# Kernel tuning notes

Hardware: AMD Instinct MI355X
Metric: run time of the kernel (lower is better)

Reference implementation:

```python
import jax, jax.numpy as jnp
import numpy as np
import math

B, L, D_MODEL, H = 2, 2048, 2048, 16
HD = D_MODEL // H  # 128


def _rope(x):
    # x: (B,H,L,HD) interleaved-pair RoPE (GPT-NeoX / RoFormer style with ::2 strides)
    hd = x.shape[-1]
    inv_freq = 1.0 / (10000.0 ** (jnp.arange(0, hd, 2, dtype=jnp.float32) / hd))  # (HD/2,)
    t = jnp.arange(x.shape[2], dtype=jnp.float32)
    freqs = t[:, None] * inv_freq[None, :]            # (L, HD/2)
    cos = jnp.cos(freqs)[None, None]                  # (1,1,L,HD/2)
    sin = jnp.sin(freqs)[None, None]
    x1 = x[..., ::2]
    x2 = x[..., 1::2]
    even = x1 * cos - x2 * sin
    odd = x1 * sin + x2 * cos
    # interleave even/odd back: (...,HD/2,2) -> (...,HD)
    return jnp.stack([even, odd], axis=-1).reshape(x.shape)


def setup_inputs() -> dict:
    key = jax.random.key(0)
    k1, k2, k3, k4, k5, k6 = jax.random.split(key, 6)
    x_q = jax.random.normal(k1, (B, L, D_MODEL), dtype=jnp.float32)
    x_kv = jax.random.normal(k2, (B, L, D_MODEL), dtype=jnp.float32)
    # causal additive mask: 0 keep, -1e9 masked, broadcastable to (B,H,L,S)
    causal = jnp.tril(jnp.ones((L, L), dtype=bool))
    attn_mask = jnp.where(causal, 0.0, -1e9).astype(jnp.float32)[None, None]
    s = 0.02
    w_q = jax.random.normal(k3, (D_MODEL, D_MODEL), dtype=jnp.float32) * s
    w_k = jax.random.normal(k4, (D_MODEL, D_MODEL), dtype=jnp.float32) * s
    w_v = jax.random.normal(k5, (D_MODEL, D_MODEL), dtype=jnp.float32) * s
    w_o = jax.random.normal(k6, (D_MODEL, D_MODEL), dtype=jnp.float32) * s
    return {"x_q": x_q, "x_kv": x_kv, "attn_mask": attn_mask,
            "w_q": w_q, "w_k": w_k, "w_v": w_v, "w_o": w_o}


def _shape(x):
    b, l, _ = x.shape
    return x.reshape(b, l, H, HD).transpose(0, 2, 1, 3)  # (B,H,L,HD)


def reference(x_q, x_kv, attn_mask, w_q, w_k, w_v, w_o):
    # torch Linear (no bias): y = x @ W.T
    q = _shape(x_q @ w_q.T)
    k = _shape(x_kv @ w_k.T)
    v = _shape(x_kv @ w_v.T)
    q = _rope(q)
    k = _rope(k)
    scale = 1.0 / math.sqrt(HD)
    scores = jnp.einsum('bhld,bhsd->bhls', q, k) * scale + attn_mask
    attn = jax.nn.softmax(scores, axis=-1)            # (B,H,L,S)
    out = jnp.einsum('bhls,bhsd->bhld', attn, v)
    out = out.transpose(0, 2, 1, 3).reshape(x_q.shape[0], x_q.shape[1], H * HD)
    out = out @ w_o.T
    return (out, attn)
```

## Files before the change

kernel.cpp:

```cpp
#include <hip/hip_runtime.h>
#include <hip/hip_bf16.h>
#include <math.h>

#define B_ 2
#define L_ 2048
#define D_ 2048
#define H_ 16
#define HD_ 128
#define E_ (B_*L_*D_)
#define W_ (D_*D_)

typedef __bf16 bf16;
typedef __bf16 bf16x8 __attribute__((ext_vector_type(8)));
typedef __bf16 bf16x4 __attribute__((ext_vector_type(4)));
typedef float  f32x4  __attribute__((ext_vector_type(4)));

#define GLL16(gp_, lp_) __builtin_amdgcn_global_load_lds( \
    (const __attribute__((address_space(1))) void*)(gp_), \
    (__attribute__((address_space(3))) void*)(lp_), 16, 0, 0)

#define BARRIER() do { asm volatile("" ::: "memory"); \
    __builtin_amdgcn_s_barrier(); \
    asm volatile("" ::: "memory"); } while (0)

#define WAITN(N) asm volatile("s_waitcnt vmcnt(" #N ")" ::: "memory")

__global__ void prep(const float* __restrict__ xq, const float* __restrict__ xkv,
                     const float* __restrict__ wq, const float* __restrict__ wk,
                     const float* __restrict__ wv, const float* __restrict__ wo,
                     bf16* __restrict__ xqb, bf16* __restrict__ xkvb,
                     bf16* __restrict__ wqb, bf16* __restrict__ wkb,
                     bf16* __restrict__ wvb, bf16* __restrict__ wob,
                     float* __restrict__ ct, float* __restrict__ st) {
  int g = blockIdx.x;
  if (g < 16384) {
    const float* s = (g < 8192) ? xq : xkv;
    bf16* d = (g < 8192) ? xqb : xkvb;
    int i = ((g & 8191) * 256 + threadIdx.x) * 4;
    f32x4 v = *reinterpret_cast<const f32x4*>(s + i);
    bf16x4 o; o[0]=(bf16)v[0]; o[1]=(bf16)v[1]; o[2]=(bf16)v[2]; o[3]=(bf16)v[3];
    *reinterpret_cast<bf16x4*>(d + i) = o;
  } else if (g < 32768) {
    int gg = g - 16384;
    int which = gg >> 12;
    const float* s = (which==0)?wq:(which==1)?wk:(which==2)?wv:wo;
    bf16* d = (which==0)?wqb:(which==1)?wkb:(which==2)?wvb:wob;
    int i = ((gg & 4095) * 256 + threadIdx.x) * 4;
    f32x4 v = *reinterpret_cast<const f32x4*>(s + i);
    bf16x4 o; o[0]=(bf16)v[0]; o[1]=(bf16)v[1]; o[2]=(bf16)v[2]; o[3]=(bf16)v[3];
    *reinterpret_cast<bf16x4*>(d + i) = o;
  } else {
    int idx = (g - 32768) * 256 + threadIdx.x;
    int t = idx >> 6, i = idx & 63;
    float inv = powf(10000.0f, -2.0f * (float)i / 128.0f);
    float f = (float)t * inv;
    ct[t * 64 + i] = cosf(f);
    st[t * 64 + i] = sinf(f);
  }
}

__global__ __launch_bounds__(256, 4) void gemm_qkv(
    const bf16* __restrict__ xq, const bf16* __restrict__ xkv,
    const bf16* __restrict__ wq, const bf16* __restrict__ wk, const bf16* __restrict__ wv,
    const float* __restrict__ ct, const float* __restrict__ st,
    bf16* __restrict__ Qo, bf16* __restrict__ Ko, bf16* __restrict__ Vt) {
  __shared__ bf16 As[128 * 64];
  __shared__ bf16 Bs[128 * 64];
  const int tid = threadIdx.x;
  const int lane = tid & 63;
  const int w = tid >> 6;
  const int l15 = lane & 15, lg = lane >> 4;
  const int which = blockIdx.x >> 4;
  const int n0 = (blockIdx.x & 15) * 128;
  const int m0 = blockIdx.y * 128;
  const int wm = (w >> 1) * 64, wn = (w & 1) * 64;
  const bf16* A  = (which == 0) ? xq : xkv;
  const bf16* Wt = (which == 0) ? wq : ((which == 1) ? wk : wv);

  int rowS[4], schS[4];
#pragma unroll
  for (int s = 0; s < 4; ++s) {
    int cl = s * 256 + tid;
    rowS[s] = cl >> 3;
    schS[s] = ((cl & 7) ^ ((cl >> 3) & 7)) << 3;
  }

  f32x4 acc[4][4];
#pragma unroll
  for (int m = 0; m < 4; ++m)
#pragma unroll
    for (int n = 0; n < 4; ++n) acc[m][n] = (f32x4){0.f, 0.f, 0.f, 0.f};

  for (int kt = 0; kt < D_; kt += 64) {
    __syncthreads();
#pragma unroll
    for (int s = 0; s < 4; ++s) {
      GLL16(A  + (size_t)(m0 + rowS[s]) * D_ + kt + schS[s], As + s * 2048 + w * 512);
      GLL16(Wt + (size_t)(n0 + rowS[s]) * D_ + kt + schS[s], Bs + s * 2048 + w * 512);
    }
    __syncthreads();
#pragma unroll
    for (int kk = 0; kk < 64; kk += 32) {
      bf16x8 af[4], bfr[4];
#pragma unroll
      for (int m = 0; m < 4; ++m)
        af[m] = *reinterpret_cast<const bf16x8*>(
            As + (wm + m * 16 + l15) * 64 + ((((kk >> 3) + lg) ^ (l15 & 7)) << 3));
#pragma unroll
      for (int n = 0; n < 4; ++n)
        bfr[n] = *reinterpret_cast<const bf16x8*>(
            Bs + (wn + n * 16 + l15) * 64 + ((((kk >> 3) + lg) ^ (l15 & 7)) << 3));
#pragma unroll
      for (int m = 0; m < 4; ++m)
#pragma unroll
        for (int n = 0; n < 4; ++n)
          acc[m][n] = __builtin_amdgcn_mfma_f32_16x16x32_bf16(af[m], bfr[n], acc[m][n], 0, 0, 0);
    }
  }

  if (which == 2) {
    const int b = m0 >> 11;
    const int l0b = (m0 & 2047) + wm + lg * 4;
#pragma unroll
    for (int m = 0; m < 4; ++m) {
      int l0 = l0b + m * 16;
#pragma unroll
      for (int n = 0; n < 4; ++n) {
        int c = n0 + wn + n * 16 + l15;
        int hd = (b * 16 + (c >> 7)) * 128 + (c & 127);
        bf16x4 o;
        o[0] = (bf16)acc[m][n][0]; o[1] = (bf16)acc[m][n][1];
        o[2] = (bf16)acc[m][n][2]; o[3] = (bf16)acc[m][n][3];
        *reinterpret_cast<bf16x4*>(Vt + (size_t)hd * L_ + l0) = o;
      }
    }
  } else {
    bf16* Out = which ? Ko : Qo;
    const bool odd = (l15 & 1);
#pragma unroll
    for (int m = 0; m < 4; ++m) {
      int row = m0 + wm + m * 16 + lg * 4;
      int l = row & 2047;
#pragma unroll
      for (int n = 0; n < 4; ++n) {
        int c = n0 + wn + n * 16 + l15;
        int i = (c & 127) >> 1;
#pragma unroll
        for (int r = 0; r < 4; ++r) {
          float own = acc[m][n][r];
          float prt = __shfl_xor(own, 1, 64);
          float cc = ct[(size_t)(l + r) * 64 + i];
          float ss = st[(size_t)(l + r) * 64 + i];
          float res = odd ? (prt * ss + own * cc) : (own * cc - prt * ss);
          Out[(size_t)(row + r) * D_ + c] = (bf16)res;
        }
      }
    }
  }
}

__global__ __launch_bounds__(256, 4) void gemm_bt(const bf16* __restrict__ A,
                                                  const bf16* __restrict__ Bw,
                                                  float* __restrict__ Cout,
                                                  int M, int N, int K) {
  __shared__ bf16 As[128 * 64];
  __shared__ bf16 Bs[128 * 64];
  const int tid = threadIdx.x;
  const int lane = tid & 63;
  const int w = tid >> 6;
  const int l15 = lane & 15, lg = lane >> 4;
  const int m0 = blockIdx.y * 128, n0 = blockIdx.x * 128;
  const int wm = (w >> 1) * 64, wn = (w & 1) * 64;

  int rowS[4], schS[4];
#pragma unroll
  for (int s = 0; s < 4; ++s) {
    int cl = s * 256 + tid;
    rowS[s] = cl >> 3;
    schS[s] = ((cl & 7) ^ ((cl >> 3) & 7)) << 3;
  }

  f32x4 acc[4][4];
#pragma unroll
  for (int m = 0; m < 4; ++m)
#pragma unroll
    for (int n = 0; n < 4; ++n) acc[m][n] = (f32x4){0.f, 0.f, 0.f, 0.f};

  for (int kt = 0; kt < K; kt += 64) {
    __syncthreads();
#pragma unroll
    for (int s = 0; s < 4; ++s) {
      GLL16(A  + (size_t)(m0 + rowS[s]) * K + kt + schS[s], As + s * 2048 + w * 512);
      GLL16(Bw + (size_t)(n0 + rowS[s]) * K + kt + schS[s], Bs + s * 2048 + w * 512);
    }
    __syncthreads();
#pragma unroll
    for (int kk = 0; kk < 64; kk += 32) {
      bf16x8 af[4], bfr[4];
#pragma unroll
      for (int m = 0; m < 4; ++m)
        af[m] = *reinterpret_cast<const bf16x8*>(
            As + (wm + m * 16 + l15) * 64 + ((((kk >> 3) + lg) ^ (l15 & 7)) << 3));
#pragma unroll
      for (int n = 0; n < 4; ++n)
        bfr[n] = *reinterpret_cast<const bf16x8*>(
            Bs + (wn + n * 16 + l15) * 64 + ((((kk >> 3) + lg) ^ (l15 & 7)) << 3));
#pragma unroll
      for (int m = 0; m < 4; ++m)
#pragma unroll
        for (int n = 0; n < 4; ++n)
          acc[m][n] = __builtin_amdgcn_mfma_f32_16x16x32_bf16(af[m], bfr[n], acc[m][n], 0, 0, 0);
    }
  }
#pragma unroll
  for (int m = 0; m < 4; ++m) {
    int orow = m0 + wm + m * 16 + lg * 4;
#pragma unroll
    for (int n = 0; n < 4; ++n) {
      int col = n0 + wn + n * 16 + l15;
#pragma unroll
      for (int r = 0; r < 4; ++r)
        Cout[(size_t)(orow + r) * N + col] = acc[m][n][r];
    }
  }
}

__global__ __launch_bounds__(256, 2) void attn_fused(const bf16* __restrict__ Qb,
                                                     const bf16* __restrict__ Kb,
                                                     const bf16* __restrict__ Vt,
                                                     float* __restrict__ attn,
                                                     bf16* __restrict__ Oh) {
  __shared__ bf16 Klds[2][64 * 128];
  __shared__ bf16 Vlds[128 * 64];
  __shared__ bf16 Plds[4][32][72];

  const int tid = threadIdx.x;
  const int w = tid >> 6, lane = tid & 63;
  const int l15 = lane & 15, lg = lane >> 4;

  int g = blockIdx.x + 16 * blockIdx.y;
  int tq, bh;
  if (g < 256) { tq = g & 15;  bh = g >> 4; }
  else { int h2 = g - 256; tq = 15 - (h2 & 15); bh = 16 + (h2 >> 4); }
  const int b = bh >> 4, h = bh & 15;

  const int q0w = tq * 128 + w * 32;
  const int ntW = (q0w >> 6) + 1;
  const int ntB = 2 * tq + 2;
  const float sc2 = 0.08838834764831845f * 1.44269504088896f;

  const bf16* kb = Kb + ((size_t)b * L_) * D_ + h * HD_;
  const bf16* vb = Vt + (size_t)bh * HD_ * L_;
  float* arow = attn + ((size_t)bh * L_ + q0w) * L_;

  bf16x8 qf[2][4];
#pragma unroll
  for (int qc = 0; qc < 2; ++qc) {
    const bf16* qrow = Qb + ((size_t)b * L_ + q0w + qc * 16 + l15) * D_ + h * HD_;
#pragma unroll
    for (int c = 0; c < 4; ++c)
      qf[qc][c] = *reinterpret_cast<const bf16x8*>(qrow + c * 32 + lg * 8);
  }

  int rK[4], sK[4], rV[4], sV[4];
#pragma unroll
  for (int s = 0; s < 4; ++s) {
    int ck = s * 256 + tid;
    rK[s] = ck >> 4; sK[s] = ((ck & 15) ^ (rK[s] & 7)) << 3;
    rV[s] = ck >> 3; sV[s] = ((ck & 7) ^ (rV[s] & 7)) << 3;
  }

  auto stageK = [&](int gp, int buf) {
#pragma unroll
    for (int s = 0; s < 4; ++s)
      GLL16(kb + (size_t)(gp * 64 + rK[s]) * D_ + sK[s],
            &Klds[0][0] + buf * 8192 + s * 2048 + w * 512);
  };
  auto stageV = [&](int gp) {
#pragma unroll
    for (int s = 0; s < 4; ++s)
      GLL16(vb + (size_t)rV[s] * L_ + gp * 64 + sV[s],
            Vlds + s * 2048 + w * 512);
  };
  auto qkt = [&](const bf16* kl, f32x4 acc[2][4]) {
#pragma unroll
    for (int c = 0; c < 4; ++c)
#pragma unroll
      for (int t = 0; t < 4; ++t) {
        bf16x8 kf = *reinterpret_cast<const bf16x8*>(
            kl + (t * 16 + l15) * 128 + ((((c << 2) + lg) ^ (l15 & 7)) << 3));
#pragma unroll
        for (int qc = 0; qc < 2; ++qc)
          acc[qc][t] = __builtin_amdgcn_mfma_f32_16x16x32_bf16(qf[qc][c], kf, acc[qc][t], 0, 0, 0);
      }
  };
  auto zstore32 = [&](int gp) {
#pragma unroll
    for (int qc = 0; qc < 2; ++qc)
#pragma unroll
      for (int t = 0; t < 4; ++t)
#pragma unroll
        for (int r = 0; r < 4; ++r)
          arow[(size_t)(qc * 16 + lg * 4 + r) * L_ + gp * 64 + t * 16 + l15] = 0.f;
  };

  float sum[2][4] = {{0.f,0.f,0.f,0.f},{0.f,0.f,0.f,0.f}};
  stageK(0, 0);
  for (int gp = 0; gp < ntB; ++gp) {
    BARRIER();
    const bool hn = (gp + 1 < ntB);
    if (hn) { stageK(gp + 1, (gp + 1) & 1); WAITN(4); }
    else    { WAITN(0); }
    BARRIER();
    if (gp < ntW) {
      f32x4 acc[2][4];
#pragma unroll
      for (int qc = 0; qc < 2; ++qc)
#pragma unroll
        for (int t = 0; t < 4; ++t) acc[qc][t] = (f32x4){0.f,0.f,0.f,0.f};
      qkt(&Klds[gp & 1][0], acc);
      if (gp < ntW - 1) {
#pragma unroll
        for (int qc = 0; qc < 2; ++qc)
#pragma unroll
          for (int t = 0; t < 4; ++t)
#pragma unroll
            for (int r = 0; r < 4; ++r)
              sum[qc][r] += exp2f(acc[qc][t][r] * sc2);
      } else {
#pragma unroll
        for (int qc = 0; qc < 2; ++qc)
#pragma unroll
          for (int t = 0; t < 4; ++t)
#pragma unroll
            for (int r = 0; r < 4; ++r) {
              int kc = gp * 64 + t * 16 + l15;
              int qr = q0w + qc * 16 + lg * 4 + r;
              sum[qc][r] += (kc <= qr) ? exp2f(acc[qc][t][r] * sc2) : 0.f;
            }
      }
    } else {
      zstore32(gp);
    }
  }
  float rinv[2][4];
#pragma unroll
  for (int qc = 0; qc < 2; ++qc)
#pragma unroll
    for (int r = 0; r < 4; ++r) {
      float s = sum[qc][r];
#pragma unroll
      for (int sh = 1; sh < 16; sh <<= 1)
        s += __shfl_xor(s, sh, 64);
      rinv[qc][r] = 1.0f / s;
    }

  f32x4 oacc[2][8];
#pragma unroll
  for (int qc = 0; qc < 2; ++qc)
#pragma unroll
    for (int i = 0; i < 8; ++i) oacc[qc][i] = (f32x4){0.f, 0.f, 0.f, 0.f};

  BARRIER();
  stageK(0, 0);
  for (int gp = 0; gp < ntB; ++gp) {
    BARRIER();
    stageV(gp);
    const bool hn = (gp + 1 < ntB);
    if (hn) stageK(gp + 1, (gp + 1) & 1);
    if (gp == 0) { WAITN(8); }
    else if (hn) { WAITN(40); }
    else         { WAITN(36); }
    BARRIER();
    const bool act = gp < ntW;
    float pv[2][4][4];
    if (act) {
      f32x4 acc[2][4];
#pragma unroll
      for (int qc = 0; qc < 2; ++qc)
#pragma unroll
        for (int t = 0; t < 4; ++t) acc[qc][t] = (f32x4){0.f,0.f,0.f,0.f};
      qkt(&Klds[gp & 1][0], acc);
      if (gp < ntW - 1) {
#pragma unroll
        for (int qc = 0; qc < 2; ++qc)
#pragma unroll
          for (int t = 0; t < 4; ++t)
#pragma unroll
            for (int r = 0; r < 4; ++r)
              pv[qc][t][r] = exp2f(acc[qc][t][r] * sc2) * rinv[qc][r];
      } else {
#pragma unroll
        for (int qc = 0; qc < 2; ++qc)
#pragma unroll
          for (int t = 0; t < 4; ++t)
#pragma unroll
            for (int r = 0; r < 4; ++r) {
              int kc = gp * 64 + t * 16 + l15;
              int qr = q0w + qc * 16 + lg * 4 + r;
              pv[qc][t][r] = (kc <= qr) ? exp2f(acc[qc][t][r] * sc2) * rinv[qc][r] : 0.f;
            }
      }
#pragma unroll
      for (int qc = 0; qc < 2; ++qc)
#pragma unroll
        for (int t = 0; t < 4; ++t)
#pragma unroll
          for (int r = 0; r < 4; ++r)
            Plds[w][qc * 16 + lg * 4 + r][t * 16 + l15] = (bf16)pv[qc][t][r];
    }
    if (hn) WAITN(4); else WAITN(0);
    if (act) {
#pragma unroll
      for (int qc = 0; qc < 2; ++qc)
#pragma unroll
        for (int t = 0; t < 4; ++t)
#pragma unroll
          for (int r = 0; r < 4; ++r)
            arow[(size_t)(qc * 16 + lg * 4 + r) * L_ + gp * 64 + t * 16 + l15] = pv[qc][t][r];
    } else {
      zstore32(gp);
    }
    BARRIER();
    if (act) {
      asm volatile("s_waitcnt lgkmcnt(0)" ::: "memory");
      __builtin_amdgcn_sched_barrier(0);
      bf16x8 pa[2][2];
#pragma unroll
      for (int qc = 0; qc < 2; ++qc)
#pragma unroll
        for (int ck = 0; ck < 2; ++ck)
          pa[qc][ck] = *reinterpret_cast<const bf16x8*>(&Plds[w][qc * 16 + l15][ck * 32 + lg * 8]);
#pragma unroll
      for (int ck = 0; ck < 2; ++ck)
#pragma unroll
        for (int t8 = 0; t8 < 8; ++t8) {
          bf16x8 vf = *reinterpret_cast<const bf16x8*>(
              Vlds + (t8 * 16 + l15) * 64 + ((((ck << 2) + lg) ^ (l15 & 7)) << 3));
#pragma unroll
          for (int qc = 0; qc < 2; ++qc)
            oacc[qc][t8] = __builtin_amdgcn_mfma_f32_16x16x32_bf16(pa[qc][ck], vf, oacc[qc][t8], 0, 0, 0);
        }
      asm volatile("s_waitcnt lgkmcnt(0)" ::: "memory");
    }
  }

  for (int gp2 = ntB; gp2 < 32; ++gp2) {
#pragma unroll
    for (int i = 0; i < 8; ++i)
      *reinterpret_cast<f32x4*>(arow + (size_t)(i * 4 + lg) * L_ + gp2 * 64 + l15 * 4)
          = (f32x4){0.f, 0.f, 0.f, 0.f};
  }

#pragma unroll
  for (int qc = 0; qc < 2; ++qc) {
    bf16* orow = Oh + ((size_t)b * L_ + q0w + qc * 16) * D_ + h * HD_;
#pragma unroll
    for (int t8 = 0; t8 < 8; ++t8)
#pragma unroll
      for (int r = 0; r < 4; ++r)
        orow[(size_t)(lg * 4 + r) * D_ + t8 * 16 + l15] = (bf16)oacc[qc][t8][r];
  }
}

extern "C" void kernel_launch(void* const* d_in, const int* in_sizes, int n_in,
                              void* d_out, int out_size, void* d_ws, size_t ws_size,
                              hipStream_t stream) {
  const float* x_q  = (const float*)d_in[0];
  const float* x_kv = (const float*)d_in[1];
  const float* w_q = (const float*)d_in[3];
  const float* w_k = (const float*)d_in[4];
  const float* w_v = (const float*)d_in[5];
  const float* w_o = (const float*)d_in[6];

  char* p = (char*)d_ws;
  auto alloc = [&](size_t bytes) { char* r = p; p += (bytes + 255) & ~(size_t)255; return r; };
  bf16* xq_b  = (bf16*)alloc((size_t)E_ * 2);
  bf16* xkv_b = (bf16*)alloc((size_t)E_ * 2);
  bf16* wq_b  = (bf16*)alloc((size_t)W_ * 2);
  bf16* wk_b  = (bf16*)alloc((size_t)W_ * 2);
  bf16* wv_b  = (bf16*)alloc((size_t)W_ * 2);
  bf16* wo_b  = (bf16*)alloc((size_t)W_ * 2);
  bf16* Qraw  = (bf16*)alloc((size_t)E_ * 2);
  bf16* Kraw  = (bf16*)alloc((size_t)E_ * 2);
  bf16* Vt    = (bf16*)alloc((size_t)E_ * 2);
  bf16* Oh    = (bf16*)alloc((size_t)E_ * 2);
  float* ct   = (float*)alloc((size_t)L_ * 64 * 4);
  float* st2  = (float*)alloc((size_t)L_ * 64 * 4);

  float* out0     = (float*)d_out;
  float* attn_out = out0 + E_;

  prep<<<33280, 256, 0, stream>>>(x_q, x_kv, w_q, w_k, w_v, w_o,
                                  xq_b, xkv_b, wq_b, wk_b, wv_b, wo_b, ct, st2);
  gemm_qkv<<<dim3(48, 32), 256, 0, stream>>>(xq_b, xkv_b, wq_b, wk_b, wv_b,
                                             ct, st2, Qraw, Kraw, Vt);
  attn_fused<<<dim3(16, 32), 256, 0, stream>>>(Qraw, Kraw, Vt, attn_out, Oh);
  gemm_bt<<<dim3(16, 32), 256, 0, stream>>>(Oh, wo_b, out0, B_*L_, D_, D_);
}
```

Measured before the change: 394.4 us.

## Double-buffer V instead of K in attention pass two and add MFMA priority

The second attention pass now double-buffers V, with K single-buffered, and prefetches the next K and V tiles after the QK^T phase so the loads overlap the P store and PV MFMAs. The pass loses one barrier per iteration. The first pass reuses the V buffer as its second K buffer, keeping LDS usage about the same while letting V stay resident across iterations. The P padding drops from 72 to 68 columns, and s_setprio raises wave priority around the MFMA loops. The changed waitcnt counts and buffer aliasing are delicate and could introduce races or LDS bank conflicts.

```diff
diff --git a/kernel.cpp b/kernel.cpp
--- a/kernel.cpp
+++ b/kernel.cpp
@@ -230,9 +230,9 @@
                                                      const bf16* __restrict__ Vt,
                                                      float* __restrict__ attn,
                                                      bf16* __restrict__ Oh) {
-  __shared__ bf16 Klds[2][64 * 128];
-  __shared__ bf16 Vlds[128 * 64];
-  __shared__ bf16 Plds[4][32][72];
+  __shared__ bf16 Klds[64 * 128];
+  __shared__ bf16 Vlds[2][128 * 64];
+  __shared__ bf16 Plds[4][32][68];
 
   const int tid = threadIdx.x;
   const int w = tid >> 6, lane = tid & 63;
@@ -270,19 +270,18 @@
     rV[s] = ck >> 3; sV[s] = ((ck & 7) ^ (rV[s] & 7)) << 3;
   }
 
-  auto stageK = [&](int gp, int buf) {
+  auto stageKto = [&](int gp, bf16* dst) {
 #pragma unroll
     for (int s = 0; s < 4; ++s)
-      GLL16(kb + (size_t)(gp * 64 + rK[s]) * D_ + sK[s],
-            &Klds[0][0] + buf * 8192 + s * 2048 + w * 512);
+      GLL16(kb + (size_t)(gp * 64 + rK[s]) * D_ + sK[s], dst + s * 2048 + w * 512);
   };
-  auto stageV = [&](int gp) {
+  auto stageV = [&](int gp, int buf) {
 #pragma unroll
     for (int s = 0; s < 4; ++s)
-      GLL16(vb + (size_t)rV[s] * L_ + gp * 64 + sV[s],
-            Vlds + s * 2048 + w * 512);
+      GLL16(vb + (size_t)rV[s] * L_ + gp * 64 + sV[s], &Vlds[buf][0] + s * 2048 + w * 512);
   };
   auto qkt = [&](const bf16* kl, f32x4 acc[2][4]) {
+    __builtin_amdgcn_s_setprio(1);
 #pragma unroll
     for (int c = 0; c < 4; ++c)
 #pragma unroll
@@ -293,6 +292,7 @@
         for (int qc = 0; qc < 2; ++qc)
           acc[qc][t] = __builtin_amdgcn_mfma_f32_16x16x32_bf16(qf[qc][c], kf, acc[qc][t], 0, 0, 0);
       }
+    __builtin_amdgcn_s_setprio(0);
   };
   auto zstore32 = [&](int gp) {
 #pragma unroll
@@ -305,12 +305,14 @@
   };
 
   float sum[2][4] = {{0.f,0.f,0.f,0.f},{0.f,0.f,0.f,0.f}};
-  stageK(0, 0);
+  stageKto(0, Klds);
   for (int gp = 0; gp < ntB; ++gp) {
     BARRIER();
     const bool hn = (gp + 1 < ntB);
-    if (hn) { stageK(gp + 1, (gp + 1) & 1); WAITN(4); }
-    else    { WAITN(0); }
+    if (hn) stageKto(gp + 1, ((gp + 1) & 1) ? &Vlds[0][0] : Klds);
+    const bool pz = (gp > 0) && ((gp - 1) >= ntW);
+    if (pz) { if (hn) WAITN(36); else WAITN(32); }
+    else    { if (hn) WAITN(4);  else WAITN(0);  }
     BARRIER();
     if (gp < ntW) {
       f32x4 acc[2][4];
@@ -318,7 +320,7 @@
       for (int qc = 0; qc < 2; ++qc)
 #pragma unroll
         for (int t = 0; t < 4; ++t) acc[qc][t] = (f32x4){0.f,0.f,0.f,0.f};
-      qkt(&Klds[gp & 1][0], acc);
+      qkt((gp & 1) ? &Vlds[0][0] : Klds, acc);
       if (gp < ntW - 1) {
 #pragma unroll
         for (int qc = 0; qc < 2; ++qc)
@@ -362,15 +364,10 @@
     for (int i = 0; i < 8; ++i) oacc[qc][i] = (f32x4){0.f, 0.f, 0.f, 0.f};
 
   BARRIER();
-  stageK(0, 0);
+  stageKto(0, Klds);
+  stageV(0, 0);
   for (int gp = 0; gp < ntB; ++gp) {
-    BARRIER();
-    stageV(gp);
-    const bool hn = (gp + 1 < ntB);
-    if (hn) stageK(gp + 1, (gp + 1) & 1);
-    if (gp == 0) { WAITN(8); }
-    else if (hn) { WAITN(40); }
-    else         { WAITN(36); }
+    if (gp == 0) { WAITN(0); } else { WAITN(32); }
     BARRIER();
     const bool act = gp < ntW;
     float pv[2][4][4];
@@ -380,7 +377,7 @@
       for (int qc = 0; qc < 2; ++qc)
 #pragma unroll
         for (int t = 0; t < 4; ++t) acc[qc][t] = (f32x4){0.f,0.f,0.f,0.f};
-      qkt(&Klds[gp & 1][0], acc);
+      qkt(Klds, acc);
       if (gp < ntW - 1) {
 #pragma unroll
         for (int qc = 0; qc < 2; ++qc)
@@ -401,6 +398,11 @@
               pv[qc][t][r] = (kc <= qr) ? exp2f(acc[qc][t][r] * sc2) * rinv[qc][r] : 0.f;
             }
       }
+    }
+    BARRIER();
+    const bool hn = (gp + 1 < ntB);
+    if (hn) { stageKto(gp + 1, Klds); stageV(gp + 1, (gp + 1) & 1); }
+    if (act) {
 #pragma unroll
       for (int qc = 0; qc < 2; ++qc)
 #pragma unroll
@@ -408,9 +410,6 @@
 #pragma unroll
           for (int r = 0; r < 4; ++r)
             Plds[w][qc * 16 + lg * 4 + r][t * 16 + l15] = (bf16)pv[qc][t][r];
-    }
-    if (hn) WAITN(4); else WAITN(0);
-    if (act) {
 #pragma unroll
       for (int qc = 0; qc < 2; ++qc)
 #pragma unroll
@@ -418,11 +417,6 @@
 #pragma unroll
           for (int r = 0; r < 4; ++r)
             arow[(size_t)(qc * 16 + lg * 4 + r) * L_ + gp * 64 + t * 16 + l15] = pv[qc][t][r];
-    } else {
-      zstore32(gp);
-    }
-    BARRIER();
-    if (act) {
       asm volatile("s_waitcnt lgkmcnt(0)" ::: "memory");
       __builtin_amdgcn_sched_barrier(0);
       bf16x8 pa[2][2];
@@ -431,17 +425,21 @@
 #pragma unroll
         for (int ck = 0; ck < 2; ++ck)
           pa[qc][ck] = *reinterpret_cast<const bf16x8*>(&Plds[w][qc * 16 + l15][ck * 32 + lg * 8]);
+      const bf16* vl = &Vlds[gp & 1][0];
+      __builtin_amdgcn_s_setprio(1);
 #pragma unroll
       for (int ck = 0; ck < 2; ++ck)
 #pragma unroll
         for (int t8 = 0; t8 < 8; ++t8) {
           bf16x8 vf = *reinterpret_cast<const bf16x8*>(
-              Vlds + (t8 * 16 + l15) * 64 + ((((ck << 2) + lg) ^ (l15 & 7)) << 3));
+              vl + (t8 * 16 + l15) * 64 + ((((ck << 2) + lg) ^ (l15 & 7)) << 3));
 #pragma unroll
           for (int qc = 0; qc < 2; ++qc)
             oacc[qc][t8] = __builtin_amdgcn_mfma_f32_16x16x32_bf16(pa[qc][ck], vf, oacc[qc][t8], 0, 0, 0);
         }
-      asm volatile("s_waitcnt lgkmcnt(0)" ::: "memory");
+      __builtin_amdgcn_s_setprio(0);
+    } else {
+      zstore32(gp);
     }
   }
 
```

Result: slower. 411.4 us (+4.3%).

## Rewrite QKV GEMM with 256x256 tiles, double-buffered LDS and ping-pong scheduling

Applied to the files above, without the earlier changes.

Replaces the 128x128 single-buffered QKV projection GEMM with a 256x256 tile kernel using 512 threads, double-buffered LDS and asynchronous global-to-LDS prefetch of the next K tile. The inner loop is split into phases using barriers, lgkmcnt waits and s_setprio so waves interleave MFMA work with LDS reads. This raises per-block data reuse and aims to hide global load latency. In exchange it uses 128KB of LDS and more accumulator registers, which lowers occupancy, and the grid drops to 384 blocks, which may underfill the GPU's compute units.

```diff
diff --git a/kernel.cpp b/kernel.cpp
--- a/kernel.cpp
+++ b/kernel.cpp
@@ -24,6 +24,8 @@
     asm volatile("" ::: "memory"); } while (0)
 
 #define WAITN(N) asm volatile("s_waitcnt vmcnt(" #N ")" ::: "memory")
+#define LGKM0SB() do { asm volatile("s_waitcnt lgkmcnt(0)" ::: "memory"); \
+    __builtin_amdgcn_sched_barrier(0); } while (0)
 
 __global__ void prep(const float* __restrict__ xq, const float* __restrict__ xkv,
                      const float* __restrict__ wq, const float* __restrict__ wk,
@@ -59,95 +61,142 @@
   }
 }
 
-__global__ __launch_bounds__(256, 4) void gemm_qkv(
+__global__ __launch_bounds__(512, 2) void gemm_qkv256(
     const bf16* __restrict__ xq, const bf16* __restrict__ xkv,
     const bf16* __restrict__ wq, const bf16* __restrict__ wk, const bf16* __restrict__ wv,
     const float* __restrict__ ct, const float* __restrict__ st,
     bf16* __restrict__ Qo, bf16* __restrict__ Ko, bf16* __restrict__ Vt) {
-  __shared__ bf16 As[128 * 64];
-  __shared__ bf16 Bs[128 * 64];
+  __shared__ bf16 Ab[2][256 * 64];
+  __shared__ bf16 Bb[2][256 * 64];
   const int tid = threadIdx.x;
-  const int lane = tid & 63;
-  const int w = tid >> 6;
+  const int w = tid >> 6, lane = tid & 63;
   const int l15 = lane & 15, lg = lane >> 4;
-  const int which = blockIdx.x >> 4;
-  const int n0 = (blockIdx.x & 15) * 128;
-  const int m0 = blockIdx.y * 128;
-  const int wm = (w >> 1) * 64, wn = (w & 1) * 64;
+  const int wm = w >> 2, wn = w & 3;
+  const int which = blockIdx.x >> 3;
+  const int n0 = (blockIdx.x & 7) * 256;
+  const int m0 = blockIdx.y * 256;
   const bf16* A  = (which == 0) ? xq : xkv;
   const bf16* Wt = (which == 0) ? wq : ((which == 1) ? wk : wv);
 
-  int rowS[4], schS[4];
+  int rS[4], cS[4];
 #pragma unroll
   for (int s = 0; s < 4; ++s) {
-    int cl = s * 256 + tid;
-    rowS[s] = cl >> 3;
-    schS[s] = ((cl & 7) ^ ((cl >> 3) & 7)) << 3;
-  }
-
-  f32x4 acc[4][4];
-#pragma unroll
-  for (int m = 0; m < 4; ++m)
-#pragma unroll
-    for (int n = 0; n < 4; ++n) acc[m][n] = (f32x4){0.f, 0.f, 0.f, 0.f};
-
-  for (int kt = 0; kt < D_; kt += 64) {
-    __syncthreads();
+    int ch = s * 512 + tid;
+    rS[s] = ch >> 3;
+    cS[s] = ((ch & 7) ^ ((ch >> 3) & 7)) << 3;
+  }
+
+  auto stage = [&](int t, int buf) {
 #pragma unroll
     for (int s = 0; s < 4; ++s) {
-      GLL16(A  + (size_t)(m0 + rowS[s]) * D_ + kt + schS[s], As + s * 2048 + w * 512);
-      GLL16(Wt + (size_t)(n0 + rowS[s]) * D_ + kt + schS[s], Bs + s * 2048 + w * 512);
-    }
-    __syncthreads();
-#pragma unroll
-    for (int kk = 0; kk < 64; kk += 32) {
-      bf16x8 af[4], bfr[4];
-#pragma unroll
-      for (int m = 0; m < 4; ++m)
-        af[m] = *reinterpret_cast<const bf16x8*>(
-            As + (wm + m * 16 + l15) * 64 + ((((kk >> 3) + lg) ^ (l15 & 7)) << 3));
+      GLL16(A  + (size_t)(m0 + rS[s]) * D_ + t * 64 + cS[s], &Ab[buf][0] + s * 4096 + w * 512);
+      GLL16(Wt + (size_t)(n0 + rS[s]) * D_ + t * 64 + cS[s], &Bb[buf][0] + s * 4096 + w * 512);
+    }
+  };
+#define RD(bufp, row, x) (*reinterpret_cast<const bf16x8*>((bufp) + (row) * 64 + (((x) ^ (l15 & 7)) << 3)))
+
+  f32x4 acc[8][4];
+#pragma unroll
+  for (int i = 0; i < 8; ++i)
+#pragma unroll
+    for (int n = 0; n < 4; ++n) acc[i][n] = (f32x4){0.f, 0.f, 0.f, 0.f};
+
+  stage(0, 0);
+  WAITN(0);
+  BARRIER();
+
+  for (int t = 0; t < 32; ++t) {
+    const bf16* Al = &Ab[t & 1][0];
+    const bf16* Bl = &Bb[t & 1][0];
+    bf16x8 af[4], bfr[4];
+    const bool hn = (t + 1 < 32);
+
+    if (hn) stage(t + 1, (t & 1) ^ 1);
+#pragma unroll
+    for (int n = 0; n < 4; ++n) bfr[n] = RD(Bl, wn * 64 + n * 16 + l15, lg);
+#pragma unroll
+    for (int i = 0; i < 4; ++i) af[i] = RD(Al, wm * 128 + i * 16 + l15, lg);
+    BARRIER(); LGKM0SB();
+    __builtin_amdgcn_s_setprio(1);
+#pragma unroll
+    for (int i = 0; i < 4; ++i)
 #pragma unroll
       for (int n = 0; n < 4; ++n)
-        bfr[n] = *reinterpret_cast<const bf16x8*>(
-            Bs + (wn + n * 16 + l15) * 64 + ((((kk >> 3) + lg) ^ (l15 & 7)) << 3));
-#pragma unroll
-      for (int m = 0; m < 4; ++m)
-#pragma unroll
-        for (int n = 0; n < 4; ++n)
-          acc[m][n] = __builtin_amdgcn_mfma_f32_16x16x32_bf16(af[m], bfr[n], acc[m][n], 0, 0, 0);
-    }
-  }
+        acc[i][n] = __builtin_amdgcn_mfma_f32_16x16x32_bf16(af[i], bfr[n], acc[i][n], 0, 0, 0);
+    __builtin_amdgcn_s_setprio(0);
+    BARRIER();
+
+#pragma unroll
+    for (int i = 0; i < 4; ++i) af[i] = RD(Al, wm * 128 + (4 + i) * 16 + l15, lg);
+    BARRIER(); LGKM0SB();
+    __builtin_amdgcn_s_setprio(1);
+#pragma unroll
+    for (int i = 0; i < 4; ++i)
+#pragma unroll
+      for (int n = 0; n < 4; ++n)
+        acc[4 + i][n] = __builtin_amdgcn_mfma_f32_16x16x32_bf16(af[i], bfr[n], acc[4 + i][n], 0, 0, 0);
+    __builtin_amdgcn_s_setprio(0);
+    BARRIER();
+
+#pragma unroll
+    for (int n = 0; n < 4; ++n) bfr[n] = RD(Bl, wn * 64 + n * 16 + l15, 4 + lg);
+#pragma unroll
+    for (int i = 0; i < 4; ++i) af[i] = RD(Al, wm * 128 + i * 16 + l15, 4 + lg);
+    BARRIER(); LGKM0SB();
+    __builtin_amdgcn_s_setprio(1);
+#pragma unroll
+    for (int i = 0; i < 4; ++i)
+#pragma unroll
+      for (int n = 0; n < 4; ++n)
+        acc[i][n] = __builtin_amdgcn_mfma_f32_16x16x32_bf16(af[i], bfr[n], acc[i][n], 0, 0, 0);
+    __builtin_amdgcn_s_setprio(0);
+    BARRIER();
+
+#pragma unroll
+    for (int i = 0; i < 4; ++i) af[i] = RD(Al, wm * 128 + (4 + i) * 16 + l15, 4 + lg);
+    BARRIER(); LGKM0SB();
+    __builtin_amdgcn_s_setprio(1);
+#pragma unroll
+    for (int i = 0; i < 4; ++i)
+#pragma unroll
+      for (int n = 0; n < 4; ++n)
+        acc[4 + i][n] = __builtin_amdgcn_mfma_f32_16x16x32_bf16(af[i], bfr[n], acc[4 + i][n], 0, 0, 0);
+    __builtin_amdgcn_s_setprio(0);
+    if (hn) WAITN(0);
+    BARRIER();
+  }
+#undef RD
 
   if (which == 2) {
     const int b = m0 >> 11;
-    const int l0b = (m0 & 2047) + wm + lg * 4;
-#pragma unroll
-    for (int m = 0; m < 4; ++m) {
-      int l0 = l0b + m * 16;
-#pragma unroll
-      for (int n = 0; n < 4; ++n) {
-        int c = n0 + wn + n * 16 + l15;
+#pragma unroll
+    for (int mi = 0; mi < 8; ++mi) {
+      int row = m0 + wm * 128 + mi * 16 + lg * 4;
+      int l = row & 2047;
+#pragma unroll
+      for (int ni = 0; ni < 4; ++ni) {
+        int c = n0 + wn * 64 + ni * 16 + l15;
         int hd = (b * 16 + (c >> 7)) * 128 + (c & 127);
         bf16x4 o;
-        o[0] = (bf16)acc[m][n][0]; o[1] = (bf16)acc[m][n][1];
-        o[2] = (bf16)acc[m][n][2]; o[3] = (bf16)acc[m][n][3];
-        *reinterpret_cast<bf16x4*>(Vt + (size_t)hd * L_ + l0) = o;
+        o[0] = (bf16)acc[mi][ni][0]; o[1] = (bf16)acc[mi][ni][1];
+        o[2] = (bf16)acc[mi][ni][2]; o[3] = (bf16)acc[mi][ni][3];
+        *reinterpret_cast<bf16x4*>(Vt + (size_t)hd * L_ + l) = o;
       }
     }
   } else {
     bf16* Out = which ? Ko : Qo;
     const bool odd = (l15 & 1);
 #pragma unroll
-    for (int m = 0; m < 4; ++m) {
-      int row = m0 + wm + m * 16 + lg * 4;
+    for (int mi = 0; mi < 8; ++mi) {
+      int row = m0 + wm * 128 + mi * 16 + lg * 4;
       int l = row & 2047;
 #pragma unroll
-      for (int n = 0; n < 4; ++n) {
-        int c = n0 + wn + n * 16 + l15;
+      for (int ni = 0; ni < 4; ++ni) {
+        int c = n0 + wn * 64 + ni * 16 + l15;
         int i = (c & 127) >> 1;
 #pragma unroll
         for (int r = 0; r < 4; ++r) {
-          float own = acc[m][n][r];
+          float own = acc[mi][ni][r];
           float prt = __shfl_xor(own, 1, 64);
           float cc = ct[(size_t)(l + r) * 64 + i];
           float ss = st[(size_t)(l + r) * 64 + i];
@@ -493,8 +542,8 @@
 
   prep<<<33280, 256, 0, stream>>>(x_q, x_kv, w_q, w_k, w_v, w_o,
                                   xq_b, xkv_b, wq_b, wk_b, wv_b, wo_b, ct, st2);
-  gemm_qkv<<<dim3(48, 32), 256, 0, stream>>>(xq_b, xkv_b, wq_b, wk_b, wv_b,
-                                             ct, st2, Qraw, Kraw, Vt);
+  gemm_qkv256<<<dim3(24, 16), 512, 0, stream>>>(xq_b, xkv_b, wq_b, wk_b, wv_b,
+                                                ct, st2, Qraw, Kraw, Vt);
   attn_fused<<<dim3(16, 32), 256, 0, stream>>>(Qraw, Kraw, Vt, attn_out, Oh);
   gemm_bt<<<dim3(16, 32), 256, 0, stream>>>(Oh, wo_b, out0, B_*L_, D_, D_);
 }
```

Result: slower. 456.3 us (+15.7%).

## Stage K tiles in pairs during softmax-sum pass using spare LDS buffers

Applied to the files above, without the earlier changes.

The first attention pass (row-sum of exponentials) now loads two 64-key K tiles per iteration. It reuses the V and P LDS buffers as extra K buffers, so four buffers are double-buffered in pairs and the number of barrier/wait rounds is halved. The zero-fill of the masked upper-triangle attention tiles is also dropped from this pass, which removes redundant global stores if the second pass already writes them. The risks are more LDS and register pressure, and incorrect attention output if those zeros are not written elsewhere.

```diff
diff --git a/kernel.cpp b/kernel.cpp
--- a/kernel.cpp
+++ b/kernel.cpp
@@ -253,6 +253,15 @@
   const bf16* vb = Vt + (size_t)bh * HD_ * L_;
   float* arow = attn + ((size_t)bh * L_ + q0w) * L_;
 
+  auto kbufp = [&](int i) -> bf16* {
+    switch (i) {
+      case 0:  return &Klds[0][0];
+      case 1:  return &Klds[1][0];
+      case 2:  return Vlds;
+      default: return (bf16*)&Plds[0][0][0];
+    }
+  };
+
   bf16x8 qf[2][4];
 #pragma unroll
   for (int qc = 0; qc < 2; ++qc) {
@@ -270,11 +279,10 @@
     rV[s] = ck >> 3; sV[s] = ((ck & 7) ^ (rV[s] & 7)) << 3;
   }
 
-  auto stageK = [&](int gp, int buf) {
+  auto stageKto = [&](int gp, bf16* dst) {
 #pragma unroll
     for (int s = 0; s < 4; ++s)
-      GLL16(kb + (size_t)(gp * 64 + rK[s]) * D_ + sK[s],
-            &Klds[0][0] + buf * 8192 + s * 2048 + w * 512);
+      GLL16(kb + (size_t)(gp * 64 + rK[s]) * D_ + sK[s], dst + s * 2048 + w * 512);
   };
   auto stageV = [&](int gp) {
 #pragma unroll
@@ -305,42 +313,51 @@
   };
 
   float sum[2][4] = {{0.f,0.f,0.f,0.f},{0.f,0.f,0.f,0.f}};
-  stageK(0, 0);
-  for (int gp = 0; gp < ntB; ++gp) {
+  const int npair = ntB >> 1;
+  stageKto(0, kbufp(0));
+  stageKto(1, kbufp(1));
+  for (int p = 0; p < npair; ++p) {
     BARRIER();
-    const bool hn = (gp + 1 < ntB);
-    if (hn) { stageK(gp + 1, (gp + 1) & 1); WAITN(4); }
-    else    { WAITN(0); }
+    const bool hn = (p + 1 < npair);
+    if (hn) {
+      stageKto(2 * p + 2, kbufp(2 * ((p + 1) & 1)));
+      stageKto(2 * p + 3, kbufp(2 * ((p + 1) & 1) + 1));
+      WAITN(8);
+    } else {
+      WAITN(0);
+    }
     BARRIER();
-    if (gp < ntW) {
-      f32x4 acc[2][4];
-#pragma unroll
-      for (int qc = 0; qc < 2; ++qc)
-#pragma unroll
-        for (int t = 0; t < 4; ++t) acc[qc][t] = (f32x4){0.f,0.f,0.f,0.f};
-      qkt(&Klds[gp & 1][0], acc);
-      if (gp < ntW - 1) {
+#pragma unroll
+    for (int half = 0; half < 2; ++half) {
+      int gp = 2 * p + half;
+      if (gp < ntW) {
+        f32x4 acc[2][4];
 #pragma unroll
         for (int qc = 0; qc < 2; ++qc)
 #pragma unroll
-          for (int t = 0; t < 4; ++t)
-#pragma unroll
-            for (int r = 0; r < 4; ++r)
-              sum[qc][r] += exp2f(acc[qc][t][r] * sc2);
-      } else {
-#pragma unroll
-        for (int qc = 0; qc < 2; ++qc)
-#pragma unroll
-          for (int t = 0; t < 4; ++t)
-#pragma unroll
-            for (int r = 0; r < 4; ++r) {
-              int kc = gp * 64 + t * 16 + l15;
-              int qr = q0w + qc * 16 + lg * 4 + r;
-              sum[qc][r] += (kc <= qr) ? exp2f(acc[qc][t][r] * sc2) : 0.f;
-            }
+          for (int t = 0; t < 4; ++t) acc[qc][t] = (f32x4){0.f,0.f,0.f,0.f};
+        qkt(kbufp(2 * (p & 1) + half), acc);
+        if (gp < ntW - 1) {
+#pragma unroll
+          for (int qc = 0; qc < 2; ++qc)
+#pragma unroll
+            for (int t = 0; t < 4; ++t)
+#pragma unroll
+              for (int r = 0; r < 4; ++r)
+                sum[qc][r] += exp2f(acc[qc][t][r] * sc2);
+        } else {
+#pragma unroll
+          for (int qc = 0; qc < 2; ++qc)
+#pragma unroll
+            for (int t = 0; t < 4; ++t)
+#pragma unroll
+              for (int r = 0; r < 4; ++r) {
+                int kc = gp * 64 + t * 16 + l15;
+                int qr = q0w + qc * 16 + lg * 4 + r;
+                sum[qc][r] += (kc <= qr) ? exp2f(acc[qc][t][r] * sc2) : 0.f;
+              }
+        }
       }
-    } else {
-      zstore32(gp);
     }
   }
   float rinv[2][4];
@@ -362,12 +379,12 @@
     for (int i = 0; i < 8; ++i) oacc[qc][i] = (f32x4){0.f, 0.f, 0.f, 0.f};
 
   BARRIER();
-  stageK(0, 0);
+  stageKto(0, &Klds[0][0]);
   for (int gp = 0; gp < ntB; ++gp) {
     BARRIER();
     stageV(gp);
     const bool hn = (gp + 1 < ntB);
-    if (hn) stageK(gp + 1, (gp + 1) & 1);
+    if (hn) stageKto(gp + 1, &Klds[(gp + 1) & 1][0]);
     if (gp == 0) { WAITN(8); }
     else if (hn) { WAITN(40); }
     else         { WAITN(36); }
```

After: 391.5 us. About the same (-0.8%).
